# Kernel optimization log

Measured on AMD Instinct MI355X. Metric: run time of the kernel, lower is better.

## Reference

```python
import jax, jax.numpy as jnp
import numpy as np

EPS = 1e-5  # torch InstanceNorm1d default

def _inorm(x):
    # instance norm over length dim per (batch, channel), no affine, biased var
    m = jnp.mean(x, axis=-1, keepdims=True)
    v = jnp.var(x, axis=-1, keepdims=True)
    return (x - m) * jax.lax.rsqrt(v + EPS)

def _conv1x1(W, b, x):
    # kernel-size-1 Conv1d == per-position linear: [O,C] x [B,C,T] -> [B,O,T]
    return jnp.einsum('oc,bct->bot', W, x) + b[None, :, None]

def setup_inputs() -> dict:
    key = jax.random.key(0)
    ks = jax.random.split(key, 10)
    B, C, T = 4, 512, 2048
    s = 1.0 / np.sqrt(C)  # conv1d default init scale
    return {
        'x_c': jax.random.normal(ks[0], (B, C, T), jnp.float32),
        'x_s': jax.random.normal(ks[1], (B, C, T), jnp.float32),
        'Wn': jax.random.normal(ks[2], (C, C), jnp.float32) * s,
        'bn': jax.random.normal(ks[3], (C,), jnp.float32) * s,
        'Wm': jax.random.normal(ks[4], (C, C), jnp.float32) * s,
        'bm': jax.random.normal(ks[5], (C,), jnp.float32) * s,
        'Wl': jax.random.normal(ks[6], (C, C), jnp.float32) * s,
        'bl': jax.random.normal(ks[7], (C,), jnp.float32) * s,
        'Wo': jax.random.normal(ks[8], (C, C), jnp.float32) * s,
        'bo': jax.random.normal(ks[9], (C,), jnp.float32) * s,
    }

def reference(x_c, x_s, Wn, bn, Wm, bm, Wl, bl, Wo, bo):
    Mn = _conv1x1(Wn, bn, _inorm(x_c))           # [B,C,Tc]
    Mm = _conv1x1(Wm, bm, _inorm(x_s))           # [B,C,Ts]
    A = jax.nn.softmax(jnp.einsum('bct,bcs->bts', Mn, Mm), axis=-1)  # [B,Tc,Ts]
    Ml = _conv1x1(Wl, bl, x_s)                   # [B,C,Ts]
    Mo = jnp.einsum('bcs,bts->bct', Ml, A)       # [B,C,Tc]
    return _conv1x1(Wo, bo, Mo) + x_c
```

## Files before the change

kernel.cpp:

```cpp
#include <hip/hip_runtime.h>
#include <hip/hip_bf16.h>
#include <stdint.h>

typedef _Float16 f16;
typedef _Float16 f16x8 __attribute__((ext_vector_type(8)));
typedef _Float16 f16x4 __attribute__((ext_vector_type(4)));
typedef float    f32x4 __attribute__((ext_vector_type(4)));

#define BB 4
#define CC 512
#define TT 2048

__device__ __forceinline__ void gload16(const void* g, void* l) {
  __builtin_amdgcn_global_load_lds((const __attribute__((address_space(1))) void*)g,
                                   (__attribute__((address_space(3))) void*)l, 16, 0, 0);
}

__global__ __launch_bounds__(256) void stats_kernel(
    const float* __restrict__ xc, const float* __restrict__ xs,
    float* __restrict__ meanc, float* __restrict__ invc,
    float* __restrict__ means, float* __restrict__ invs) {
  const int c = blockIdx.x, b = blockIdx.y, which = blockIdx.z;
  const float* src = (which ? xs : xc) + ((long)b * CC + c) * TT;
  const int tid = threadIdx.x;
  const float4* p4 = (const float4*)src;
  float4 a = p4[tid * 2], d = p4[tid * 2 + 1];
  float s = a.x + a.y + a.z + a.w + d.x + d.y + d.z + d.w;
  float q = a.x*a.x + a.y*a.y + a.z*a.z + a.w*a.w + d.x*d.x + d.y*d.y + d.z*d.z + d.w*d.w;
  #pragma unroll
  for (int o = 32; o; o >>= 1) { s += __shfl_xor(s, o); q += __shfl_xor(q, o); }
  __shared__ float sred[4], qred[4];
  if ((tid & 63) == 0) { sred[tid >> 6] = s; qred[tid >> 6] = q; }
  __syncthreads();
  if (tid == 0) {
    float S = sred[0] + sred[1] + sred[2] + sred[3];
    float Q = qred[0] + qred[1] + qred[2] + qred[3];
    float mean = S * (1.f / TT);
    float var  = Q * (1.f / TT) - mean * mean;
    float inv  = 1.0f / sqrtf(var + 1e-5f);
    float* mp = which ? means : meanc;
    float* ip = which ? invs  : invc;
    mp[b * CC + c] = mean;
    ip[b * CC + c] = inv;
  }
}

__global__ __launch_bounds__(256) void transpose_kernel(
    const float* __restrict__ xc, const float* __restrict__ xs,
    f16* __restrict__ xcT, f16* __restrict__ xsT) {
  const int b = blockIdx.z & 3, which = blockIdx.z >> 2;
  const float* src = (which ? xs : xc) + (long)b * CC * TT;
  f16* dst = (which ? xsT : xcT) + (long)b * TT * CC;
  const int t0 = blockIdx.x * 64, c0 = blockIdx.y * 64;
  __shared__ float tile[64][65];
  const int tid = threadIdx.x;
  #pragma unroll
  for (int it = 0; it < 4; ++it) {
    int s = it * 256 + tid, r = s >> 4, q = s & 15;
    float4 v = *(const float4*)&src[(long)(c0 + r) * TT + t0 + q * 4];
    tile[r][q*4+0] = v.x; tile[r][q*4+1] = v.y; tile[r][q*4+2] = v.z; tile[r][q*4+3] = v.w;
  }
  __syncthreads();
  #pragma unroll
  for (int it = 0; it < 4; ++it) {
    int s = it * 256 + tid, r = s >> 4, q = s & 15;
    f16x4 o;
    o[0] = (f16)tile[q*4+0][r]; o[1] = (f16)tile[q*4+1][r];
    o[2] = (f16)tile[q*4+2][r]; o[3] = (f16)tile[q*4+3][r];
    *(f16x4*)&dst[(long)(t0 + r) * CC + c0 + q * 4] = o;
  }
}

__global__ __launch_bounds__(256) void prepw_kernel(
    const float* __restrict__ W, const float* __restrict__ bias,
    const float* __restrict__ mean, const float* __restrict__ inv,
    f16* __restrict__ Weff, float* __restrict__ beff) {
  const int o = blockIdx.x, b = blockIdx.y, tid = threadIdx.x;
  float acc = 0.f;
  #pragma unroll
  for (int j = 0; j < 2; ++j) {
    int c = tid + j * 256;
    float iv = inv[b * CC + c];
    float wv = W[(long)o * CC + c] * iv;
    Weff[((long)b * CC + o) * CC + c] = (f16)wv;
    acc += wv * mean[b * CC + c];
  }
  #pragma unroll
  for (int off = 32; off; off >>= 1) acc += __shfl_xor(acc, off);
  __shared__ float red[4];
  if ((tid & 63) == 0) red[tid >> 6] = acc;
  __syncthreads();
  if (tid == 0) beff[b * CC + o] = bias[o] - (red[0] + red[1] + red[2] + red[3]);
}

__global__ __launch_bounds__(256) void f2h_kernel(const float* __restrict__ src,
                                                  f16* __restrict__ dst) {
  long i = ((long)blockIdx.x * 256 + threadIdx.x) * 8;
  float4 a = *(const float4*)&src[i], d = *(const float4*)&src[i + 4];
  f16x8 o;
  o[0]=(f16)a.x; o[1]=(f16)a.y; o[2]=(f16)a.z; o[3]=(f16)a.w;
  o[4]=(f16)d.x; o[5]=(f16)d.y; o[6]=(f16)d.z; o[7]=(f16)d.w;
  *(f16x8*)&dst[i] = o;
}

__global__ __launch_bounds__(256) void softmax_kernel(float* __restrict__ S) {
  float* p = S + ((long)blockIdx.y * TT + blockIdx.x) * TT;
  const int tid = threadIdx.x;
  float4 a = ((const float4*)p)[tid * 2], d = ((const float4*)p)[tid * 2 + 1];
  float v[8] = {a.x, a.y, a.z, a.w, d.x, d.y, d.z, d.w};
  float m = v[0];
  #pragma unroll
  for (int j = 1; j < 8; ++j) m = fmaxf(m, v[j]);
  #pragma unroll
  for (int o = 32; o; o >>= 1) m = fmaxf(m, __shfl_xor(m, o));
  __shared__ float red[4], red2[4];
  if (!(tid & 63)) red[tid >> 6] = m;
  __syncthreads();
  m = fmaxf(fmaxf(red[0], red[1]), fmaxf(red[2], red[3]));
  float e[8], sum = 0.f;
  #pragma unroll
  for (int j = 0; j < 8; ++j) { e[j] = __expf(v[j] - m); sum += e[j]; }
  #pragma unroll
  for (int o = 32; o; o >>= 1) sum += __shfl_xor(sum, o);
  if (!(tid & 63)) red2[tid >> 6] = sum;
  __syncthreads();
  sum = red2[0] + red2[1] + red2[2] + red2[3];
  float is = 1.f / sum;
  f16x8 o8;
  #pragma unroll
  for (int j = 0; j < 8; ++j) o8[j] = (f16)(e[j] * is);
  ((f16x8*)p)[tid] = o8;
}

template <typename OutT, bool TRANSW, bool BIAS, bool RESID>
__global__ __launch_bounds__(256) void gemm_kernel(
    const f16* __restrict__ A, long long sAb, int lda,
    const f16* __restrict__ BT, long long sBb, int ldb,
    OutT* __restrict__ C, long long sCb, int ldc,
    const float* __restrict__ bias, long long sBiasb,
    const float* __restrict__ resid, long long sResb, int ldres,
    int K) {
  const int b = blockIdx.z;
  A += (long long)b * sAb; BT += (long long)b * sBb; C += (long long)b * sCb;
  if (BIAS) bias += (long long)b * sBiasb;
  if (RESID) resid += (long long)b * sResb;
  const int bm = blockIdx.y * 128, bn = blockIdx.x * 128;
  const int tid = threadIdx.x, lane = tid & 63, wv = tid >> 6;
  const int wr = wv >> 1, wc = wv & 1;

  __shared__ f16 sA[128 * 32];
  __shared__ f16 sB[128 * 32];

  const int rS = lane >> 2, cS = lane & 3;
  const char* gA0 = (const char*)(A + (long)(bm + (wv*2+0)*16 + rS) * lda + cS * 8);
  const char* gA1 = (const char*)(A + (long)(bm + (wv*2+1)*16 + rS) * lda + cS * 8);
  const char* gB0 = (const char*)(BT + (long)(bn + (wv*2+0)*16 + rS) * ldb + cS * 8);
  const char* gB1 = (const char*)(BT + (long)(bn + (wv*2+1)*16 + rS) * ldb + cS * 8);
  char* lA0 = (char*)sA + (wv*2+0)*1024;
  char* lA1 = (char*)sA + (wv*2+1)*1024;
  char* lB0 = (char*)sB + (wv*2+0)*1024;
  char* lB1 = (char*)sB + (wv*2+1)*1024;

  const int lm = lane & 15, lk = (lane >> 4) * 8;
  f32x4 acc[4][4] = {};

  const int nk = K >> 5;
  for (int kt = 0; kt < nk; ++kt) {
    if (kt) __syncthreads();
    gload16(gA0 + (long)kt*64, lA0);
    gload16(gA1 + (long)kt*64, lA1);
    gload16(gB0 + (long)kt*64, lB0);
    gload16(gB1 + (long)kt*64, lB1);
    __syncthreads();
    f16x8 af[4], bfr[4];
    #pragma unroll
    for (int mi = 0; mi < 4; ++mi)
      af[mi] = *(const f16x8*)&sA[(wr*64 + mi*16 + lm)*32 + lk];
    #pragma unroll
    for (int ni = 0; ni < 4; ++ni)
      bfr[ni] = *(const f16x8*)&sB[(wc*64 + ni*16 + lm)*32 + lk];
    #pragma unroll
    for (int mi = 0; mi < 4; ++mi)
      #pragma unroll
      for (int ni = 0; ni < 4; ++ni)
        acc[mi][ni] = __builtin_amdgcn_mfma_f32_16x16x32_f16(af[mi], bfr[ni], acc[mi][ni], 0, 0, 0);
  }

  const int rr = (lane >> 4) * 4;
  #pragma unroll
  for (int mi = 0; mi < 4; ++mi) {
    int m0 = bm + wr*64 + mi*16 + rr;
    #pragma unroll
    for (int ni = 0; ni < 4; ++ni) {
      int n0 = bn + wc*64 + ni*16 + lm;
      f32x4 v = acc[mi][ni];
      #pragma unroll
      for (int r = 0; r < 4; ++r) {
        float val = v[r];
        if (BIAS)  val += bias[m0 + r];
        if (RESID) val += resid[(long)(m0 + r) * ldres + n0];
        if (TRANSW) C[(long)n0 * ldc + m0 + r] = (OutT)val;
        else        C[(long)(m0 + r) * ldc + n0] = (OutT)val;
      }
    }
  }
}

extern "C" void kernel_launch(void* const* d_in, const int* in_sizes, int n_in,
                              void* d_out, int out_size, void* d_ws, size_t ws_size,
                              hipStream_t stream) {
  const float* x_c = (const float*)d_in[0];
  const float* x_s = (const float*)d_in[1];
  const float* Wn  = (const float*)d_in[2];
  const float* bn  = (const float*)d_in[3];
  const float* Wm  = (const float*)d_in[4];
  const float* bm  = (const float*)d_in[5];
  const float* Wl  = (const float*)d_in[6];
  const float* bl  = (const float*)d_in[7];
  const float* Wo  = (const float*)d_in[8];
  const float* bo  = (const float*)d_in[9];
  float* out = (float*)d_out;

  char* w = (char*)d_ws;
  auto alloc = [&](size_t bytes) { char* p = w; w += (bytes + 255) & ~(size_t)255; return p; };
  float* meanc = (float*)alloc(BB * CC * 4);
  float* invc  = (float*)alloc(BB * CC * 4);
  float* means = (float*)alloc(BB * CC * 4);
  float* invs  = (float*)alloc(BB * CC * 4);
  float* bnE   = (float*)alloc(BB * CC * 4);
  float* bmE   = (float*)alloc(BB * CC * 4);
  f16* WnE = (f16*)alloc((size_t)BB * CC * CC * 2);
  f16* WmE = (f16*)alloc((size_t)BB * CC * CC * 2);
  f16* WlB = (f16*)alloc((size_t)CC * CC * 2);
  f16* WoB = (f16*)alloc((size_t)CC * CC * 2);
  f16* xcT = (f16*)alloc((size_t)BB * TT * CC * 2);
  f16* xsT = (f16*)alloc((size_t)BB * TT * CC * 2);
  f16* MnT = (f16*)alloc((size_t)BB * TT * CC * 2);
  f16* MmT = (f16*)alloc((size_t)BB * TT * CC * 2);
  f16* Ml  = (f16*)alloc((size_t)BB * CC * TT * 2);
  float* S  = (float*)alloc((size_t)BB * TT * TT * 4);
  f16* MoT = (f16*)alloc((size_t)BB * TT * CC * 2);

  dim3 blk(256);

  stats_kernel<<<dim3(CC, BB, 2), blk, 0, stream>>>(x_c, x_s, meanc, invc, means, invs);
  transpose_kernel<<<dim3(TT / 64, CC / 64, BB * 2), blk, 0, stream>>>(x_c, x_s, xcT, xsT);
  prepw_kernel<<<dim3(CC, BB), blk, 0, stream>>>(Wn, bn, meanc, invc, WnE, bnE);
  prepw_kernel<<<dim3(CC, BB), blk, 0, stream>>>(Wm, bm, means, invs, WmE, bmE);
  f2h_kernel<<<dim3(CC * CC / (256 * 8)), blk, 0, stream>>>(Wl, WlB);
  f2h_kernel<<<dim3(CC * CC / (256 * 8)), blk, 0, stream>>>(Wo, WoB);

  gemm_kernel<f16, true, true, false><<<dim3(16, 4, BB), blk, 0, stream>>>(
      WnE, (long long)CC * CC, CC, xcT, (long long)TT * CC, CC,
      MnT, (long long)TT * CC, CC, bnE, CC, nullptr, 0, 0, CC);
  gemm_kernel<f16, true, true, false><<<dim3(16, 4, BB), blk, 0, stream>>>(
      WmE, (long long)CC * CC, CC, xsT, (long long)TT * CC, CC,
      MmT, (long long)TT * CC, CC, bmE, CC, nullptr, 0, 0, CC);
  gemm_kernel<f16, false, true, false><<<dim3(16, 4, BB), blk, 0, stream>>>(
      WlB, 0, CC, xsT, (long long)TT * CC, CC,
      Ml, (long long)CC * TT, TT, bl, 0, nullptr, 0, 0, CC);
  gemm_kernel<float, false, false, false><<<dim3(16, 16, BB), blk, 0, stream>>>(
      MnT, (long long)TT * CC, CC, MmT, (long long)TT * CC, CC,
      S, (long long)TT * TT, TT, nullptr, 0, nullptr, 0, 0, CC);
  softmax_kernel<<<dim3(TT, BB), blk, 0, stream>>>(S);
  gemm_kernel<f16, false, false, false><<<dim3(4, 16, BB), blk, 0, stream>>>(
      (const f16*)S, (long long)TT * 2 * TT, 2 * TT, Ml, (long long)CC * TT, TT,
      MoT, (long long)TT * CC, CC, nullptr, 0, nullptr, 0, 0, TT);
  gemm_kernel<float, false, true, true><<<dim3(16, 4, BB), blk, 0, stream>>>(
      WoB, 0, CC, MoT, (long long)TT * CC, CC,
      out, (long long)CC * TT, TT, bo, 0, x_c, (long long)CC * TT, TT, CC);
}
```

Before: 268.9 us.

## Double-buffer GEMM with swizzled LDS, 512-thread blocks, and merged conv launches

Replaces the templated GEMM with a shared core that uses 64-wide K tiles and double-buffered LDS, so the next tile's global-to-LDS load overlaps the current tile's MFMAs. It also XOR-swizzles LDS columns to avoid bank conflicts and moves to 512-thread blocks with 8 waves of 32x64 output each. The transposed epilogue now writes packed 4-element vectors. The three 1x1-conv GEMMs are merged into one launch covering 12 z-slices. The cost is more LDS per block (64 KB) and more registers per thread, which can lower occupancy.

```diff
diff --git a/kernel.cpp b/kernel.cpp
--- a/kernel.cpp
+++ b/kernel.cpp
@@ -38,10 +38,8 @@
     float mean = S * (1.f / TT);
     float var  = Q * (1.f / TT) - mean * mean;
     float inv  = 1.0f / sqrtf(var + 1e-5f);
-    float* mp = which ? means : meanc;
-    float* ip = which ? invs  : invc;
-    mp[b * CC + c] = mean;
-    ip[b * CC + c] = inv;
+    (which ? means : meanc)[b * CC + c] = mean;
+    (which ? invs  : invc )[b * CC + c] = inv;
   }
 }
 
@@ -132,78 +130,157 @@
   ((f16x8*)p)[tid] = o8;
 }
 
-template <typename OutT, bool TRANSW, bool BIAS, bool RESID>
-__global__ __launch_bounds__(256) void gemm_kernel(
-    const f16* __restrict__ A, long long sAb, int lda,
-    const f16* __restrict__ BT, long long sBb, int ldb,
-    OutT* __restrict__ C, long long sCb, int ldc,
-    const float* __restrict__ bias, long long sBiasb,
-    const float* __restrict__ resid, long long sResb, int ldres,
-    int K) {
-  const int b = blockIdx.z;
-  A += (long long)b * sAb; BT += (long long)b * sBb; C += (long long)b * sCb;
-  if (BIAS) bias += (long long)b * sBiasb;
-  if (RESID) resid += (long long)b * sResb;
-  const int bm = blockIdx.y * 128, bn = blockIdx.x * 128;
+template <typename OutT>
+__device__ __forceinline__ void gemm_core(
+    const f16* __restrict__ A, int lda,
+    const f16* __restrict__ BT, int ldb,
+    OutT* __restrict__ C, int ldc,
+    const float* __restrict__ bias,
+    const float* __restrict__ resid, int ldres,
+    int bm, int bn, int K, bool transw) {
+
+  __shared__ f16 sA[2][128 * 64];
+  __shared__ f16 sB[2][128 * 64];
+
   const int tid = threadIdx.x, lane = tid & 63, wv = tid >> 6;
   const int wr = wv >> 1, wc = wv & 1;
 
-  __shared__ f16 sA[128 * 32];
-  __shared__ f16 sB[128 * 32];
-
-  const int rS = lane >> 2, cS = lane & 3;
-  const char* gA0 = (const char*)(A + (long)(bm + (wv*2+0)*16 + rS) * lda + cS * 8);
-  const char* gA1 = (const char*)(A + (long)(bm + (wv*2+1)*16 + rS) * lda + cS * 8);
-  const char* gB0 = (const char*)(BT + (long)(bn + (wv*2+0)*16 + rS) * ldb + cS * 8);
-  const char* gB1 = (const char*)(BT + (long)(bn + (wv*2+1)*16 + rS) * ldb + cS * 8);
-  char* lA0 = (char*)sA + (wv*2+0)*1024;
-  char* lA1 = (char*)sA + (wv*2+1)*1024;
-  char* lB0 = (char*)sB + (wv*2+0)*1024;
-  char* lB1 = (char*)sB + (wv*2+1)*1024;
-
-  const int lm = lane & 15, lk = (lane >> 4) * 8;
-  f32x4 acc[4][4] = {};
-
-  const int nk = K >> 5;
+  const int srow  = tid >> 3;
+  const int scolb = (tid & 7) * 16;
+  const int sgcolb = scolb ^ ((srow & 7) << 4);
+  const char* gA  = (const char*)A  + (long)(bm + srow) * lda * 2 + sgcolb;
+  const char* gA2 = gA + (long)64 * lda * 2;
+  const char* gB  = (const char*)BT + (long)(bn + srow) * ldb * 2 + sgcolb;
+  const char* gB2 = gB + (long)64 * ldb * 2;
+  char* lA  = (char*)&sA[0][0] + tid * 16;
+  char* lB  = (char*)&sB[0][0] + tid * 16;
+
+  const int lm = lane & 15, lkb = (lane >> 4) * 16, sw = (lane & 7) << 4;
+  int aoff[2][2], boff[4][2];
+  #pragma unroll
+  for (int mi = 0; mi < 2; ++mi) {
+    int r = wr * 32 + mi * 16 + lm;
+    #pragma unroll
+    for (int kk = 0; kk < 2; ++kk)
+      aoff[mi][kk] = r * 128 + ((kk * 64 + lkb) ^ sw);
+  }
+  #pragma unroll
+  for (int ni = 0; ni < 4; ++ni) {
+    int r = wc * 64 + ni * 16 + lm;
+    #pragma unroll
+    for (int kk = 0; kk < 2; ++kk)
+      boff[ni][kk] = r * 128 + ((kk * 64 + lkb) ^ sw);
+  }
+
+  f32x4 acc[2][4] = {};
+  const int nk = K >> 6;
+
+  {
+    gload16(gA, lA); gload16(gA2, lA + 8192);
+    gload16(gB, lB); gload16(gB2, lB + 8192);
+  }
+  __syncthreads();
+
+  int cur = 0;
   for (int kt = 0; kt < nk; ++kt) {
-    if (kt) __syncthreads();
-    gload16(gA0 + (long)kt*64, lA0);
-    gload16(gA1 + (long)kt*64, lA1);
-    gload16(gB0 + (long)kt*64, lB0);
-    gload16(gB1 + (long)kt*64, lB1);
+    if (kt + 1 < nk) {
+      long kb = (long)(kt + 1) * 128;
+      int nb = (cur ^ 1) * 16384;
+      gload16(gA + kb, lA + nb); gload16(gA2 + kb, lA + nb + 8192);
+      gload16(gB + kb, lB + nb); gload16(gB2 + kb, lB + nb + 8192);
+    }
+    const char* pa = (const char*)&sA[cur][0];
+    const char* pb = (const char*)&sB[cur][0];
+    f16x8 af[2][2], bf[4][2];
+    #pragma unroll
+    for (int mi = 0; mi < 2; ++mi)
+      #pragma unroll
+      for (int kk = 0; kk < 2; ++kk)
+        af[mi][kk] = *(const f16x8*)(pa + aoff[mi][kk]);
+    #pragma unroll
+    for (int ni = 0; ni < 4; ++ni)
+      #pragma unroll
+      for (int kk = 0; kk < 2; ++kk)
+        bf[ni][kk] = *(const f16x8*)(pb + boff[ni][kk]);
+    #pragma unroll
+    for (int kk = 0; kk < 2; ++kk)
+      #pragma unroll
+      for (int mi = 0; mi < 2; ++mi)
+        #pragma unroll
+        for (int ni = 0; ni < 4; ++ni)
+          acc[mi][ni] = __builtin_amdgcn_mfma_f32_16x16x32_f16(af[mi][kk], bf[ni][kk], acc[mi][ni], 0, 0, 0);
     __syncthreads();
-    f16x8 af[4], bfr[4];
-    #pragma unroll
-    for (int mi = 0; mi < 4; ++mi)
-      af[mi] = *(const f16x8*)&sA[(wr*64 + mi*16 + lm)*32 + lk];
-    #pragma unroll
-    for (int ni = 0; ni < 4; ++ni)
-      bfr[ni] = *(const f16x8*)&sB[(wc*64 + ni*16 + lm)*32 + lk];
-    #pragma unroll
-    for (int mi = 0; mi < 4; ++mi)
-      #pragma unroll
-      for (int ni = 0; ni < 4; ++ni)
-        acc[mi][ni] = __builtin_amdgcn_mfma_f32_16x16x32_f16(af[mi], bfr[ni], acc[mi][ni], 0, 0, 0);
-  }
-
+    cur ^= 1;
+  }
+
+  struct alignas(4 * sizeof(OutT)) Pack4 { OutT v[4]; };
   const int rr = (lane >> 4) * 4;
   #pragma unroll
-  for (int mi = 0; mi < 4; ++mi) {
-    int m0 = bm + wr*64 + mi*16 + rr;
+  for (int mi = 0; mi < 2; ++mi) {
+    int m0 = bm + wr * 32 + mi * 16 + rr;
     #pragma unroll
     for (int ni = 0; ni < 4; ++ni) {
-      int n0 = bn + wc*64 + ni*16 + lm;
+      int n0 = bn + wc * 64 + ni * 16 + lm;
       f32x4 v = acc[mi][ni];
+      float vals[4];
       #pragma unroll
       for (int r = 0; r < 4; ++r) {
-        float val = v[r];
-        if (BIAS)  val += bias[m0 + r];
-        if (RESID) val += resid[(long)(m0 + r) * ldres + n0];
-        if (TRANSW) C[(long)n0 * ldc + m0 + r] = (OutT)val;
-        else        C[(long)(m0 + r) * ldc + n0] = (OutT)val;
+        vals[r] = v[r];
+        if (bias)  vals[r] += bias[m0 + r];
+        if (resid) vals[r] += resid[(long)(m0 + r) * ldres + n0];
+      }
+      if (transw) {
+        Pack4 pk;
+        #pragma unroll
+        for (int r = 0; r < 4; ++r) pk.v[r] = (OutT)vals[r];
+        *(Pack4*)&C[(long)n0 * ldc + m0] = pk;
+      } else {
+        #pragma unroll
+        for (int r = 0; r < 4; ++r)
+          C[(long)(m0 + r) * ldc + n0] = (OutT)vals[r];
       }
     }
   }
+}
+
+__global__ __launch_bounds__(512) void conv_kernel(
+    const f16* __restrict__ xcT, const f16* __restrict__ xsT,
+    const f16* __restrict__ WnE, const float* __restrict__ bnE,
+    const f16* __restrict__ WmE, const float* __restrict__ bmE,
+    const f16* __restrict__ WlB, const float* __restrict__ bl,
+    f16* __restrict__ MnT, f16* __restrict__ MmT, f16* __restrict__ Ml) {
+  const int z = blockIdx.z, cid = z >> 2, b = z & 3;
+  const f16* A; const float* bias; const f16* B; f16* C; int ldc; bool transw;
+  if (cid == 0)      { A = WnE + (long)b*CC*CC; bias = bnE + b*CC; B = xcT + (long)b*TT*CC; C = MnT + (long)b*TT*CC; ldc = CC; transw = true; }
+  else if (cid == 1) { A = WmE + (long)b*CC*CC; bias = bmE + b*CC; B = xsT + (long)b*TT*CC; C = MmT + (long)b*TT*CC; ldc = CC; transw = true; }
+  else               { A = WlB;                 bias = bl;         B = xsT + (long)b*TT*CC; C = Ml  + (long)b*CC*TT; ldc = TT; transw = false; }
+  gemm_core<f16>(A, CC, B, CC, C, ldc, bias, nullptr, 0,
+                 blockIdx.y * 128, blockIdx.x * 128, CC, transw);
+}
+
+__global__ __launch_bounds__(512) void sgemm_kernel(
+    const f16* __restrict__ MnT, const f16* __restrict__ MmT, float* __restrict__ S) {
+  const int b = blockIdx.z;
+  gemm_core<float>(MnT + (long)b*TT*CC, CC, MmT + (long)b*TT*CC, CC,
+                   S + (long)b*TT*TT, TT, nullptr, nullptr, 0,
+                   blockIdx.y * 128, blockIdx.x * 128, CC, false);
+}
+
+__global__ __launch_bounds__(512) void pv_kernel(
+    const f16* __restrict__ P, const f16* __restrict__ Ml, f16* __restrict__ MoT) {
+  const int b = blockIdx.z;
+  gemm_core<f16>(P + (long)b*TT*2*TT, 2*TT, Ml + (long)b*CC*TT, TT,
+                 MoT + (long)b*TT*CC, CC, nullptr, nullptr, 0,
+                 blockIdx.y * 128, blockIdx.x * 128, TT, false);
+}
+
+__global__ __launch_bounds__(512) void out_kernel(
+    const f16* __restrict__ WoB, const f16* __restrict__ MoT,
+    const float* __restrict__ bo, const float* __restrict__ xc, float* __restrict__ out) {
+  const int b = blockIdx.z;
+  gemm_core<float>(WoB, CC, MoT + (long)b*TT*CC, CC,
+                   out + (long)b*CC*TT, TT, bo, xc + (long)b*CC*TT, TT,
+                   blockIdx.y * 128, blockIdx.x * 128, CC, false);
 }
 
 extern "C" void kernel_launch(void* const* d_in, const int* in_sizes, int n_in,
@@ -241,32 +318,17 @@
   float* S  = (float*)alloc((size_t)BB * TT * TT * 4);
   f16* MoT = (f16*)alloc((size_t)BB * TT * CC * 2);
 
-  dim3 blk(256);
-
-  stats_kernel<<<dim3(CC, BB, 2), blk, 0, stream>>>(x_c, x_s, meanc, invc, means, invs);
-  transpose_kernel<<<dim3(TT / 64, CC / 64, BB * 2), blk, 0, stream>>>(x_c, x_s, xcT, xsT);
-  prepw_kernel<<<dim3(CC, BB), blk, 0, stream>>>(Wn, bn, meanc, invc, WnE, bnE);
-  prepw_kernel<<<dim3(CC, BB), blk, 0, stream>>>(Wm, bm, means, invs, WmE, bmE);
-  f2h_kernel<<<dim3(CC * CC / (256 * 8)), blk, 0, stream>>>(Wl, WlB);
-  f2h_kernel<<<dim3(CC * CC / (256 * 8)), blk, 0, stream>>>(Wo, WoB);
-
-  gemm_kernel<f16, true, true, false><<<dim3(16, 4, BB), blk, 0, stream>>>(
-      WnE, (long long)CC * CC, CC, xcT, (long long)TT * CC, CC,
-      MnT, (long long)TT * CC, CC, bnE, CC, nullptr, 0, 0, CC);
-  gemm_kernel<f16, true, true, false><<<dim3(16, 4, BB), blk, 0, stream>>>(
-      WmE, (long long)CC * CC, CC, xsT, (long long)TT * CC, CC,
-      MmT, (long long)TT * CC, CC, bmE, CC, nullptr, 0, 0, CC);
-  gemm_kernel<f16, false, true, false><<<dim3(16, 4, BB), blk, 0, stream>>>(
-      WlB, 0, CC, xsT, (long long)TT * CC, CC,
-      Ml, (long long)CC * TT, TT, bl, 0, nullptr, 0, 0, CC);
-  gemm_kernel<float, false, false, false><<<dim3(16, 16, BB), blk, 0, stream>>>(
-      MnT, (long long)TT * CC, CC, MmT, (long long)TT * CC, CC,
-      S, (long long)TT * TT, TT, nullptr, 0, nullptr, 0, 0, CC);
-  softmax_kernel<<<dim3(TT, BB), blk, 0, stream>>>(S);
-  gemm_kernel<f16, false, false, false><<<dim3(4, 16, BB), blk, 0, stream>>>(
-      (const f16*)S, (long long)TT * 2 * TT, 2 * TT, Ml, (long long)CC * TT, TT,
-      MoT, (long long)TT * CC, CC, nullptr, 0, nullptr, 0, 0, TT);
-  gemm_kernel<float, false, true, true><<<dim3(16, 4, BB), blk, 0, stream>>>(
-      WoB, 0, CC, MoT, (long long)TT * CC, CC,
-      out, (long long)CC * TT, TT, bo, 0, x_c, (long long)CC * TT, TT, CC);
-}
+  stats_kernel<<<dim3(CC, BB, 2), dim3(256), 0, stream>>>(x_c, x_s, meanc, invc, means, invs);
+  transpose_kernel<<<dim3(TT / 64, CC / 64, BB * 2), dim3(256), 0, stream>>>(x_c, x_s, xcT, xsT);
+  prepw_kernel<<<dim3(CC, BB), dim3(256), 0, stream>>>(Wn, bn, meanc, invc, WnE, bnE);
+  prepw_kernel<<<dim3(CC, BB), dim3(256), 0, stream>>>(Wm, bm, means, invs, WmE, bmE);
+  f2h_kernel<<<dim3(CC * CC / (256 * 8)), dim3(256), 0, stream>>>(Wl, WlB);
+  f2h_kernel<<<dim3(CC * CC / (256 * 8)), dim3(256), 0, stream>>>(Wo, WoB);
+
+  conv_kernel<<<dim3(16, 4, 12), dim3(512), 0, stream>>>(
+      xcT, xsT, WnE, bnE, WmE, bmE, WlB, bl, MnT, MmT, Ml);
+  sgemm_kernel<<<dim3(16, 16, BB), dim3(512), 0, stream>>>(MnT, MmT, S);
+  softmax_kernel<<<dim3(TT, BB), dim3(256), 0, stream>>>(S);
+  pv_kernel<<<dim3(4, 16, BB), dim3(512), 0, stream>>>((const f16*)S, Ml, MoT);
+  out_kernel<<<dim3(16, 4, BB), dim3(512), 0, stream>>>(WoB, MoT, bo, x_c, out);
+}
```

Result: faster. 239.5 us (-10.9%).
